# Performance work log

Measured on AMD Instinct MI355X. Metric: run time of the kernel, lower is better.

Reference implementation:

```python
import jax, jax.numpy as jnp
import numpy as np

B, S, H = 1, 4096, 2048
HQ, HKV, D = 8, 4, 256
WIN = 1024          # sliding window
SOFTCAP = 50.0      # attn logit softcapping
EPS = 1e-6          # rms_norm_eps
ROPE_THETA = 10000.0


def setup_inputs() -> dict:
    key = jax.random.key(0)
    ks = jax.random.split(key, 6)
    hidden_states = jax.random.normal(ks[0], (B, S, H), dtype=jnp.float32)
    # RoPE cos/sin tables, shape [B, S, D]
    inv_freq = 1.0 / (ROPE_THETA ** (jnp.arange(0, D, 2, dtype=jnp.float32) / D))
    pos = jnp.arange(S, dtype=jnp.float32)
    freqs = pos[:, None] * inv_freq[None, :]          # [S, D/2]
    emb = jnp.concatenate([freqs, freqs], axis=-1)    # [S, D]
    cos = jnp.broadcast_to(jnp.cos(emb)[None], (B, S, D)).astype(jnp.float32)
    sin = jnp.broadcast_to(jnp.sin(emb)[None], (B, S, D)).astype(jnp.float32)
    qpos = jnp.arange(S)[:, None]
    kpos = jnp.arange(S)[None, :]
    diff = qpos - kpos
    allowed = (diff >= 0) & (diff < WIN)
    attention_mask = jnp.where(allowed, 0.0, -1e9).astype(jnp.float32)[None, None]
    attention_mask = jnp.broadcast_to(attention_mask, (B, 1, S, S))
    w_scale = 0.02
    Wq = jax.random.normal(ks[1], (HQ * D, H), dtype=jnp.float32) * w_scale
    Wk = jax.random.normal(ks[2], (HKV * D, H), dtype=jnp.float32) * w_scale
    Wv = jax.random.normal(ks[3], (HKV * D, H), dtype=jnp.float32) * w_scale
    Wo = jax.random.normal(ks[4], (H, HQ * D), dtype=jnp.float32) * w_scale
    q_norm_w = jnp.ones((D,), dtype=jnp.float32)
    k_norm_w = jnp.ones((D,), dtype=jnp.float32)
    return {"hidden_states": hidden_states, "cos": cos, "sin": sin,
            "attention_mask": attention_mask, "Wq": Wq, "Wk": Wk, "Wv": Wv,
            "Wo": Wo, "q_norm_w": q_norm_w, "k_norm_w": k_norm_w}


def _rms_norm(x, weight=None):
    # Gemma4 RMSNorm in fp32: x * rsqrt(mean(x^2) + eps) [* weight]
    ms = jnp.mean(x * x, axis=-1, keepdims=True) + EPS
    y = x * jax.lax.rsqrt(ms)
    return y * weight if weight is not None else y


def _rope(x, cos, sin):
    # x: [B,S,Hn,D]; cos/sin: [B,S,D] -> unsqueeze at dim 2
    x1, x2 = jnp.split(x, 2, axis=-1)
    rot = jnp.concatenate([-x2, x1], axis=-1)
    return x * cos[:, :, None, :] + rot * sin[:, :, None, :]


def reference(hidden_states, cos, sin, attention_mask, Wq, Wk, Wv, Wo, q_norm_w, k_norm_w):
    n_rep = HQ // HKV
    q = (hidden_states @ Wq.T).reshape(B, S, HQ, D)     # [B,S,HQ,D]
    q = _rms_norm(q, q_norm_w)
    q = _rope(q, cos, sin).transpose(0, 2, 1, 3)        # [B,HQ,S,D]
    k = (hidden_states @ Wk.T).reshape(B, S, HKV, D)
    k = _rms_norm(k, k_norm_w)
    k = _rope(k, cos, sin).transpose(0, 2, 1, 3)        # [B,HKV,S,D]
    v = (hidden_states @ Wv.T).reshape(B, S, HKV, D)
    v = _rms_norm(v).transpose(0, 2, 1, 3)              # [B,HKV,S,D]
    # repeat_kv (GQA)
    k = jnp.repeat(k, n_rep, axis=1)                    # [B,HQ,S,D]
    v = jnp.repeat(v, n_rep, axis=1)
    scores = jnp.einsum('bhqd,bhkd->bhqk', q, k)        # scaling = 1.0
    scores = jnp.tanh(scores / SOFTCAP) * SOFTCAP       # softcap
    scores = scores + attention_mask
    attn = jax.nn.softmax(scores.astype(jnp.float32), axis=-1).astype(q.dtype)
    out = jnp.einsum('bhqk,bhkd->bhqd', attn, v)        # [B,HQ,S,D]
    out = out.transpose(0, 2, 1, 3).reshape(B, S, HQ * D)
    return out @ Wo.T                                   # [B,S,H]
```

## Files before the change

kernel.cpp:

```cpp
#include <hip/hip_runtime.h>

#define S_LEN 4096
#define HID   2048
#define NHQ   8
#define NKV   4
#define DHEAD 256
#define WIN   1024

typedef __attribute__((ext_vector_type(4))) float     floatx4;
typedef __attribute__((ext_vector_type(8))) _Float16  halfx8;
typedef __attribute__((ext_vector_type(8))) __bf16    bf16x8;

__device__ __forceinline__ unsigned short f2h(float f){
  union { _Float16 h; unsigned short u; } cv; cv.h = (_Float16)f; return cv.u;
}
__device__ __forceinline__ float h2f(unsigned short u){
  union { unsigned short u; _Float16 h; } cv; cv.u = u; return (float)cv.h;
}
__device__ __forceinline__ unsigned short f2bf(float f){
  unsigned int u = __float_as_uint(f);
  u += 0x7FFFu + ((u >> 16) & 1u);
  return (unsigned short)(u >> 16);
}

__device__ __forceinline__ void gld_lds16(const void* g, void* l){
  __builtin_amdgcn_global_load_lds((const __attribute__((address_space(1))) void*)g,
                                   (__attribute__((address_space(3))) void*)l, 16, 0, 0);
}

__global__ __launch_bounds__(256) void cvt_all(const float* __restrict__ hs,
                                               const float* __restrict__ Wq,
                                               const float* __restrict__ Wk,
                                               const float* __restrict__ Wv,
                                               const float* __restrict__ Wo,
                                               unsigned short* __restrict__ h_h,
                                               unsigned short* __restrict__ w_qkv,
                                               unsigned short* __restrict__ wo){
  int bid = blockIdx.x;
  const float* src;
  unsigned short* dst;
  size_t i;
  if (bid < 8192){
    i = ((size_t)bid * 256 + threadIdx.x) * 4;
    src = hs + i; dst = h_h + i;
  } else if (bid < 16384){
    i = ((size_t)(bid - 8192) * 256 + threadIdx.x) * 4;
    int row = (int)(i >> 11), col = (int)(i & 2047);
    src = ((row < 2048) ? (Wq + ((size_t)row << 11))
         : (row < 3072) ? (Wk + ((size_t)(row - 2048) << 11))
                        : (Wv + ((size_t)(row - 3072) << 11))) + col;
    dst = w_qkv + i;
  } else {
    i = ((size_t)(bid - 16384) * 256 + threadIdx.x) * 4;
    src = Wo + i; dst = wo + i;
  }
  float4 v = *(const float4*)src;
  *(ushort4*)dst = make_ushort4(f2h(v.x), f2h(v.y), f2h(v.z), f2h(v.w));
}

template<int OUT_F32>
__global__ __launch_bounds__(512, 2) void gemm_qkv8(const unsigned short* __restrict__ A,
                                                    const unsigned short* __restrict__ B,
                                                    void* __restrict__ Cv,
                                                    int ldC, int K, int nx){
  __shared__ __align__(16) unsigned short As[2][256 * 64];
  __shared__ __align__(16) unsigned short Bs[2][256 * 64];
  const int T = K >> 6;
  const int t0 = threadIdx.x, w = t0 >> 6, lane = t0 & 63;
  const int wm = w >> 2, wn = w & 3;
  const int quad = lane >> 4, l15 = lane & 15;
  const int r7 = l15 & 7;

  const int bid = (int)blockIdx.x;
  const int by = bid / nx, bx = bid - by * nx;
  const int bm0 = by * 256, bn0 = bx * 256;

  const int grow = lane >> 3;
  const int sg8  = (((lane & 7) ^ grow) << 3);

#define STGH(U, HALF)                                                          \
  {                                                                            \
    const int sl_ = (U) & 1;                                                   \
    const unsigned short* src_ = ((HALF) < 2)                                  \
        ? (A + (size_t)(bm0 + (((HALF) & 1) << 7)) * K)                        \
        : (B + (size_t)(bn0 + (((HALF) & 1) << 7)) * K);                       \
    unsigned short* dst_ = (((HALF) < 2) ? &As[sl_][0] : &Bs[sl_][0])          \
                           + ((((HALF) & 1) << 7) * 64);                       \
    _Pragma("unroll")                                                          \
    for (int L = 0; L < 2; ++L){                                               \
      const int ck = L * 8 + w;                                                \
      gld_lds16(src_ + (size_t)((ck << 3) + grow) * K + (size_t)(U) * 64 + sg8,\
                dst_ + ck * 512);                                              \
    }                                                                          \
  }

#define LDA(MI, KS) (*(const halfx8*)&Ap[(wm*128 + (MI)*16 + l15) * 64 + ((((KS)*4 + quad) ^ r7) << 3)])
#define LDB(NI, KS) (*(const halfx8*)&Bp[(wn*64  + (NI)*16 + l15) * 64 + ((((KS)*4 + quad) ^ r7) << 3)])

  STGH(0, 0) STGH(0, 1) STGH(0, 2) STGH(0, 3)
  asm volatile("s_waitcnt vmcnt(0)" ::: "memory");
  __builtin_amdgcn_s_barrier();

  const floatx4 zf = {0.f, 0.f, 0.f, 0.f};
  floatx4 acc[8][4];
#pragma unroll
  for (int mi = 0; mi < 8; ++mi)
#pragma unroll
    for (int ni = 0; ni < 4; ++ni) acc[mi][ni] = zf;

  for (int t = 0; t < T; ++t){
    const int cur = t & 1;
    const unsigned short* Ap = &As[cur][0];
    const unsigned short* Bp = &Bs[cur][0];
    const bool pf = (t + 1 < T);
    halfx8 af[4], bf0[4], bf1[4];

#pragma unroll
    for (int mi = 0; mi < 4; ++mi) af[mi] = LDA(mi, 0);
#pragma unroll
    for (int ni = 0; ni < 4; ++ni){ bf0[ni] = LDB(ni, 0); bf1[ni] = LDB(ni, 1); }
    if (pf) STGH(t + 1, 0)
    __builtin_amdgcn_s_barrier();
    asm volatile("s_waitcnt lgkmcnt(0)" ::: "memory");
    __builtin_amdgcn_sched_barrier(0);
    __builtin_amdgcn_s_setprio(1);
#pragma unroll
    for (int mi = 0; mi < 4; ++mi)
#pragma unroll
      for (int ni = 0; ni < 4; ++ni)
        acc[mi][ni] = __builtin_amdgcn_mfma_f32_16x16x32_f16(af[mi], bf0[ni], acc[mi][ni], 0, 0, 0);
    __builtin_amdgcn_s_setprio(0);
    __builtin_amdgcn_s_barrier();
    __builtin_amdgcn_sched_barrier(0);

#pragma unroll
    for (int mi = 0; mi < 4; ++mi) af[mi] = LDA(4 + mi, 0);
    if (pf) STGH(t + 1, 1)
    __builtin_amdgcn_s_barrier();
    asm volatile("s_waitcnt lgkmcnt(0)" ::: "memory");
    __builtin_amdgcn_sched_barrier(0);
    __builtin_amdgcn_s_setprio(1);
#pragma unroll
    for (int mi = 0; mi < 4; ++mi)
#pragma unroll
      for (int ni = 0; ni < 4; ++ni)
        acc[4 + mi][ni] = __builtin_amdgcn_mfma_f32_16x16x32_f16(af[mi], bf0[ni], acc[4 + mi][ni], 0, 0, 0);
    __builtin_amdgcn_s_setprio(0);
    __builtin_amdgcn_s_barrier();
    __builtin_amdgcn_sched_barrier(0);

#pragma unroll
    for (int mi = 0; mi < 4; ++mi) af[mi] = LDA(mi, 1);
    if (pf) STGH(t + 1, 2)
    __builtin_amdgcn_s_barrier();
    asm volatile("s_waitcnt lgkmcnt(0)" ::: "memory");
    __builtin_amdgcn_sched_barrier(0);
    __builtin_amdgcn_s_setprio(1);
#pragma unroll
    for (int mi = 0; mi < 4; ++mi)
#pragma unroll
      for (int ni = 0; ni < 4; ++ni)
        acc[mi][ni] = __builtin_amdgcn_mfma_f32_16x16x32_f16(af[mi], bf1[ni], acc[mi][ni], 0, 0, 0);
    __builtin_amdgcn_s_setprio(0);
    __builtin_amdgcn_s_barrier();
    __builtin_amdgcn_sched_barrier(0);

#pragma unroll
    for (int mi = 0; mi < 4; ++mi) af[mi] = LDA(4 + mi, 1);
    if (pf) STGH(t + 1, 3)
    __builtin_amdgcn_s_barrier();
    asm volatile("s_waitcnt lgkmcnt(0)" ::: "memory");
    __builtin_amdgcn_sched_barrier(0);
    __builtin_amdgcn_s_setprio(1);
#pragma unroll
    for (int mi = 0; mi < 4; ++mi)
#pragma unroll
      for (int ni = 0; ni < 4; ++ni)
        acc[4 + mi][ni] = __builtin_amdgcn_mfma_f32_16x16x32_f16(af[mi], bf1[ni], acc[4 + mi][ni], 0, 0, 0);
    __builtin_amdgcn_s_setprio(0);
    if (pf) { asm volatile("s_waitcnt vmcnt(0)" ::: "memory"); }
    __builtin_amdgcn_s_barrier();
    __builtin_amdgcn_sched_barrier(0);
  }
#undef STGH
#undef LDA
#undef LDB

#pragma unroll
  for (int mi = 0; mi < 8; ++mi)
#pragma unroll
    for (int ni = 0; ni < 4; ++ni)
#pragma unroll
      for (int r = 0; r < 4; ++r){
        int m = bm0 + wm*128 + mi*16 + quad*4 + r;
        int n = bn0 + wn*64 + ni*16 + l15;
        float v = acc[mi][ni][r];
        if (OUT_F32) ((float*)Cv)[(size_t)m * ldC + n] = v;
        else         ((unsigned short*)Cv)[(size_t)m * ldC + n] = f2h(v);
      }
}

__global__ __launch_bounds__(256) void qkv_post(const unsigned short* __restrict__ qkvh,
                                                const float* __restrict__ cosb,
                                                const float* __restrict__ sinb,
                                                const float* __restrict__ qnw,
                                                const float* __restrict__ knw,
                                                unsigned short* __restrict__ Qf,
                                                unsigned short* __restrict__ Kf,
                                                unsigned short* __restrict__ Vf){
  int gw   = blockIdx.x * 4 + (threadIdx.x >> 6);
  int lane = threadIdx.x & 63;
  int hh = gw & 15, s = gw >> 4;
  int colbase = (hh < 8) ? hh * 256 : (hh < 12 ? 2048 + (hh - 8) * 256 : 3072 + (hh - 12) * 256);

  ushort4 raw = *(const ushort4*)(qkvh + (size_t)s * 4096 + colbase + lane * 4);
  float x0 = h2f(raw.x), x1 = h2f(raw.y), x2 = h2f(raw.z), x3 = h2f(raw.w);
  float ss = x0*x0 + x1*x1 + x2*x2 + x3*x3;
#pragma unroll
  for (int off = 32; off; off >>= 1) ss += __shfl_xor(ss, off);
  float inv = rsqrtf(ss * (1.0f / 256.0f) + 1e-6f);

  if (hh < 12){
    const float* wp = (hh < 8) ? qnw : knw;
    float4 wv = *(const float4*)(wp + lane * 4);
    float y[4] = { x0*inv*wv.x, x1*inv*wv.y, x2*inv*wv.z, x3*inv*wv.w };
    float4 cv = *(const float4*)(cosb + (size_t)s * 256 + lane * 4);
    float4 sv = *(const float4*)(sinb + (size_t)s * 256 + lane * 4);
    float cj[4] = {cv.x, cv.y, cv.z, cv.w};
    float sj[4] = {sv.x, sv.y, sv.z, sv.w};
    unsigned short oh[4];
#pragma unroll
    for (int j = 0; j < 4; ++j){
      float oth = __shfl_xor(y[j], 32);
      float rot = (lane < 32) ? -oth : oth;
      oh[j] = f2h(y[j] * cj[j] + rot * sj[j]);
    }
    ushort4 r = make_ushort4(oh[0], oh[1], oh[2], oh[3]);
    if (hh < 8) *(ushort4*)(Qf + (size_t)(hh       * S_LEN + s) * DHEAD + lane * 4) = r;
    else        *(ushort4*)(Kf + (size_t)((hh - 8) * S_LEN + s) * DHEAD + lane * 4) = r;
  } else {
    ushort4 r = make_ushort4(f2bf(x0*inv), f2bf(x1*inv), f2bf(x2*inv), f2bf(x3*inv));
    *(ushort4*)(Vf + (size_t)((hh - 12) * S_LEN + s) * DHEAD + lane * 4) = r;
  }
}

__global__ __launch_bounds__(256) void transpose_v(const unsigned short* __restrict__ v,
                                                   unsigned short* __restrict__ vt){
  __shared__ unsigned short tile[64][68];
  int kv = blockIdx.z, d0 = blockIdx.x * 64, s0 = blockIdx.y * 64;
  int t = threadIdx.x;
  int r = t >> 4, c4 = (t & 15) * 4;
#pragma unroll
  for (int i = 0; i < 4; ++i){
    int row = r + i * 16;
    ushort4 xx = *(const ushort4*)(v + (size_t)(kv * S_LEN + s0 + row) * DHEAD + d0 + c4);
    tile[row][c4] = xx.x; tile[row][c4+1] = xx.y; tile[row][c4+2] = xx.z; tile[row][c4+3] = xx.w;
  }
  __syncthreads();
#pragma unroll
  for (int i = 0; i < 4; ++i){
    int dr = r + i * 16;
    ushort4 yy = make_ushort4(tile[c4][dr], tile[c4+1][dr], tile[c4+2][dr], tile[c4+3][dr]);
    *(ushort4*)(vt + (size_t)(kv * DHEAD + d0 + dr) * S_LEN + s0 + c4) = yy;
  }
}

__global__ __launch_bounds__(256, 1) void attn_win(const unsigned short* __restrict__ Qg,
                                                   const unsigned short* __restrict__ Kg,
                                                   const unsigned short* __restrict__ Vt,
                                                   unsigned short* __restrict__ Og){
  __shared__ __align__(16) unsigned short Ks[2][8 * 32 * 32];
  __shared__ __align__(16) unsigned short Vts[2][256 * 32];
  __shared__ __align__(16) unsigned short Pb[4][32 * 40];

  const int bid = blockIdx.x;
  const int h = bid & 7, kv = h >> 1;
  const int q0 = (bid >> 3) * 128;
  const int t = threadIdx.x, w = t >> 6, lane = t & 63;
  const int quad = lane >> 4, l15 = lane & 15;
  const int l2 = lane >> 2;
  const int gsw = (((lane & 3) ^ ((l2 >> 1) & 3)) << 3);
  const int qsw = ((quad ^ ((l15 >> 1) & 3)) << 3);
  const int qw0 = q0 + w * 32;

  halfx8 qf[2][8];
#pragma unroll
  for (int s = 0; s < 2; ++s)
#pragma unroll
    for (int c = 0; c < 8; ++c)
      qf[s][c] = *(const halfx8*)(Qg + (size_t)(h * S_LEN + qw0 + s*16 + l15) * DHEAD + c*32 + quad*8);

  const floatx4 zf = {0.f, 0.f, 0.f, 0.f};
  floatx4 oacc[2][16];
#pragma unroll
  for (int s = 0; s < 2; ++s)
#pragma unroll
    for (int dt = 0; dt < 16; ++dt) oacc[s][dt] = zf;
  float l_part[2][4] = {{0.f,0.f,0.f,0.f},{0.f,0.f,0.f,0.f}};

  int kt_lo = q0 / 32 - 32; if (kt_lo < 0) kt_lo = 0;
  int kt_hi = q0 / 32 + 3;

  const size_t kbase = (size_t)kv * S_LEN * DHEAD;
  const size_t vbase = (size_t)kv * DHEAD * S_LEN;

#define STAGE(KT, B)                                                              \
  {                                                                               \
    const int key0_ = (KT) * 32;                                                  \
    _Pragma("unroll")                                                             \
    for (int j = 0; j < 4; ++j){                                                  \
      int ch = j * 4 + w;                                                         \
      int krow = (ch & 1) * 16 + l2;                                              \
      int cb = ch >> 1;                                                           \
      gld_lds16(Kg + kbase + (size_t)(key0_ + krow) * DHEAD + cb * 32 + gsw,      \
                &Ks[B][ch * 512]);                                                \
      int drow = ch * 16 + l2;                                                    \
      gld_lds16(Vt + vbase + (size_t)drow * S_LEN + key0_ + gsw,                  \
                &Vts[B][ch * 512]);                                               \
    }                                                                             \
  }

  STAGE(kt_lo, 0);

  for (int kt = kt_lo; kt <= kt_hi; ++kt){
    const int cur = (kt - kt_lo) & 1;
    if (kt < kt_hi){
      STAGE(kt + 1, cur ^ 1);
      asm volatile("s_waitcnt vmcnt(8)" ::: "memory");
    } else {
      asm volatile("s_waitcnt vmcnt(0)" ::: "memory");
    }
    __builtin_amdgcn_s_barrier();

    const int key0 = kt * 32;
    if (key0 <= qw0 + 31 && key0 + 31 >= qw0 - (WIN - 1)){
      floatx4 sc[2][2];
      sc[0][0] = zf; sc[0][1] = zf; sc[1][0] = zf; sc[1][1] = zf;
      __builtin_amdgcn_s_setprio(1);
#pragma unroll
      for (int c = 0; c < 8; ++c){
#pragma unroll
        for (int nt = 0; nt < 2; ++nt){
          halfx8 kf = *(const halfx8*)&Ks[cur][c * 1024 + (nt*16 + l15) * 32 + qsw];
          sc[0][nt] = __builtin_amdgcn_mfma_f32_16x16x32_f16(qf[0][c], kf, sc[0][nt], 0, 0, 0);
          sc[1][nt] = __builtin_amdgcn_mfma_f32_16x16x32_f16(qf[1][c], kf, sc[1][nt], 0, 0, 0);
        }
      }
      __builtin_amdgcn_s_setprio(0);
      const bool tfull = (key0 + 31 <= qw0) && (qw0 + 31 - key0 < WIN);
#pragma unroll
      for (int s = 0; s < 2; ++s)
#pragma unroll
        for (int nt = 0; nt < 2; ++nt)
#pragma unroll
          for (int r = 0; r < 4; ++r){
            float v = sc[s][nt][r];
            float e  = __builtin_amdgcn_exp2f(v * 0.0577078016f);
            float tt = __builtin_amdgcn_rcpf(e + 1.0f);
            float p  = __builtin_amdgcn_exp2f(fmaf(tt, -144.26950408f, 28.8539008f));
            if (!tfull){
              int qi = qw0 + s*16 + quad*4 + r;
              int ki = key0 + nt*16 + l15;
              p = ((ki <= qi) && (qi - ki < WIN)) ? p : 0.0f;
            }
            l_part[s][r] += p;
            Pb[w][(s*16 + quad*4 + r) * 40 + nt*16 + l15] = f2bf(p);
          }
      bf16x8 pf0 = *(const bf16x8*)&Pb[w][l15 * 40 + quad * 8];
      bf16x8 pf1 = *(const bf16x8*)&Pb[w][(16 + l15) * 40 + quad * 8];
      __builtin_amdgcn_s_setprio(1);
#pragma unroll
      for (int dt = 0; dt < 16; ++dt){
        bf16x8 vf = *(const bf16x8*)&Vts[cur][(dt*16 + l15) * 32 + qsw];
        oacc[0][dt] = __builtin_amdgcn_mfma_f32_16x16x32_bf16(pf0, vf, oacc[0][dt], 0, 0, 0);
        oacc[1][dt] = __builtin_amdgcn_mfma_f32_16x16x32_bf16(pf1, vf, oacc[1][dt], 0, 0, 0);
      }
      __builtin_amdgcn_s_setprio(0);
    }
    __builtin_amdgcn_s_barrier();
  }
#undef STAGE

#pragma unroll
  for (int s = 0; s < 2; ++s)
#pragma unroll
    for (int r = 0; r < 4; ++r){
      float l = l_part[s][r];
      l += __shfl_xor(l, 1);
      l += __shfl_xor(l, 2);
      l += __shfl_xor(l, 4);
      l += __shfl_xor(l, 8);
      float rl = 1.0f / l;
      int srow = qw0 + s*16 + quad*4 + r;
#pragma unroll
      for (int dt = 0; dt < 16; ++dt)
        Og[(size_t)srow * (NHQ * DHEAD) + h * DHEAD + dt*16 + l15] = f2h(oacc[s][dt][r] * rl);
    }
}

extern "C" void kernel_launch(void* const* d_in, const int* in_sizes, int n_in,
                              void* d_out, int out_size, void* d_ws, size_t ws_size,
                              hipStream_t stream){
  const float* hs   = (const float*)d_in[0];
  const float* cosb = (const float*)d_in[1];
  const float* sinb = (const float*)d_in[2];
  const float* Wq   = (const float*)d_in[4];
  const float* Wk   = (const float*)d_in[5];
  const float* Wv   = (const float*)d_in[6];
  const float* Wo   = (const float*)d_in[7];
  const float* qnw  = (const float*)d_in[8];
  const float* knw  = (const float*)d_in[9];
  float* out = (float*)d_out;

  const size_t MB = 1024ull * 1024ull;
  char* ws = (char*)d_ws;
  unsigned short* h_h   = (unsigned short*)(ws);
  unsigned short* w_qkv = (unsigned short*)(ws + 16 * MB);
  unsigned short* wo    = (unsigned short*)(ws + 32 * MB);
  unsigned short* qkvh  = (unsigned short*)(ws + 40 * MB);
  unsigned short* Qf    = (unsigned short*)(ws);
  unsigned short* Kf    = (unsigned short*)(ws + 16 * MB);
  unsigned short* Vf    = (unsigned short*)(ws + 24 * MB);
  unsigned short* vt    = (unsigned short*)(ws + 40 * MB);
  unsigned short* ob    = (unsigned short*)(ws + 48 * MB);

  cvt_all<<<20480, 256, 0, stream>>>(hs, Wq, Wk, Wv, Wo, h_h, w_qkv, wo);

  gemm_qkv8<0><<<256, 512, 0, stream>>>(h_h, w_qkv, qkvh, 4096, 2048, 16);

  qkv_post<<<16384, 256, 0, stream>>>(qkvh, cosb, sinb, qnw, knw, Qf, Kf, Vf);
  transpose_v<<<dim3(4, 64, 4), 256, 0, stream>>>(Vf, vt);

  attn_win<<<256, 256, 0, stream>>>(Qf, Kf, vt, ob);

  gemm_qkv8<1><<<128, 512, 0, stream>>>(ob, wo, out, 2048, 2048, 8);
}
```

Baseline: 431.0 us.

## Split attention key range across two blocks and merge partial outputs

The windowed attention kernel is split along the key dimension: each query tile is handled by two blocks covering halves of the key tiles, giving 512 blocks instead of 256 to fill more CUs. Each half writes a normalized fp16 output plus its row sums, and a new merge kernel combines them weighted by the row sums. Because softmax uses a fixed max (softcap bound), the partials can be merged without rescaling. A fallback 512-thread attention variant is used when workspace is small. The cost is an extra kernel launch and an extra round trip of the attention output through memory.

```diff
diff --git a/kernel.cpp b/kernel.cpp
--- a/kernel.cpp
+++ b/kernel.cpp
@@ -265,17 +265,20 @@
   }
 }
 
-__global__ __launch_bounds__(256, 1) void attn_win(const unsigned short* __restrict__ Qg,
-                                                   const unsigned short* __restrict__ Kg,
-                                                   const unsigned short* __restrict__ Vt,
-                                                   unsigned short* __restrict__ Og){
+__global__ __launch_bounds__(256, 1) void attn_sp(const unsigned short* __restrict__ Qg,
+                                                  const unsigned short* __restrict__ Kg,
+                                                  const unsigned short* __restrict__ Vt,
+                                                  unsigned short* __restrict__ Oh,
+                                                  float* __restrict__ lh){
   __shared__ __align__(16) unsigned short Ks[2][8 * 32 * 32];
   __shared__ __align__(16) unsigned short Vts[2][256 * 32];
   __shared__ __align__(16) unsigned short Pb[4][32 * 40];
 
   const int bid = blockIdx.x;
   const int h = bid & 7, kv = h >> 1;
-  const int q0 = (bid >> 3) * 128;
+  const int rest = bid >> 3;
+  const int q0 = (rest >> 1) * 128;
+  const int half = rest & 1;
   const int t = threadIdx.x, w = t >> 6, lane = t & 63;
   const int quad = lane >> 4, l15 = lane & 15;
   const int l2 = lane >> 2;
@@ -298,8 +301,11 @@
     for (int dt = 0; dt < 16; ++dt) oacc[s][dt] = zf;
   float l_part[2][4] = {{0.f,0.f,0.f,0.f},{0.f,0.f,0.f,0.f}};
 
-  int kt_lo = q0 / 32 - 32; if (kt_lo < 0) kt_lo = 0;
-  int kt_hi = q0 / 32 + 3;
+  int lo = q0 / 32 - 32; if (lo < 0) lo = 0;
+  const int hi = q0 / 32 + 3;
+  const int mid = lo + ((hi - lo + 2) >> 1);
+  const int lo_h = half ? mid : lo;
+  const int hi_h = half ? hi : mid - 1;
 
   const size_t kbase = (size_t)kv * S_LEN * DHEAD;
   const size_t vbase = (size_t)kv * DHEAD * S_LEN;
@@ -320,11 +326,11 @@
     }                                                                             \
   }
 
-  STAGE(kt_lo, 0);
-
-  for (int kt = kt_lo; kt <= kt_hi; ++kt){
-    const int cur = (kt - kt_lo) & 1;
-    if (kt < kt_hi){
+  STAGE(lo_h, 0);
+
+  for (int kt = lo_h; kt <= hi_h; ++kt){
+    const int cur = (kt - lo_h) & 1;
+    if (kt < hi_h){
       STAGE(kt + 1, cur ^ 1);
       asm volatile("s_waitcnt vmcnt(8)" ::: "memory");
     } else {
@@ -381,6 +387,7 @@
   }
 #undef STAGE
 
+  const size_t obase = (size_t)half * (8ull << 20);
 #pragma unroll
   for (int s = 0; s < 2; ++s)
 #pragma unroll
@@ -390,12 +397,154 @@
       l += __shfl_xor(l, 2);
       l += __shfl_xor(l, 4);
       l += __shfl_xor(l, 8);
-      float rl = 1.0f / l;
+      float rl = (l > 0.f) ? (1.0f / l) : 0.f;
       int srow = qw0 + s*16 + quad*4 + r;
+      if (l15 == 0) lh[((size_t)half * NHQ + h) * S_LEN + srow] = l;
 #pragma unroll
       for (int dt = 0; dt < 16; ++dt)
-        Og[(size_t)srow * (NHQ * DHEAD) + h * DHEAD + dt*16 + l15] = f2h(oacc[s][dt][r] * rl);
+        Oh[obase + (size_t)srow * (NHQ * DHEAD) + h * DHEAD + dt*16 + l15] = f2h(oacc[s][dt][r] * rl);
     }
+}
+
+__global__ __launch_bounds__(256) void merge_o(unsigned short* __restrict__ Oab,
+                                               const float* __restrict__ lh){
+  size_t i = ((size_t)blockIdx.x * 256 + threadIdx.x) * 4;
+  int row = (int)(i >> 11);
+  int h   = (int)((i & 2047) >> 8);
+  float a = lh[(size_t)h * S_LEN + row];
+  float b = lh[((size_t)NHQ + h) * S_LEN + row];
+  float wsum = 1.0f / (a + b);
+  float wa = a * wsum, wb = b * wsum;
+  ushort4 xa = *(const ushort4*)(Oab + i);
+  ushort4 xb = *(const ushort4*)(Oab + (8ull << 20) + i);
+  ushort4 o = make_ushort4(
+    f2h(h2f(xa.x) * wa + h2f(xb.x) * wb),
+    f2h(h2f(xa.y) * wa + h2f(xb.y) * wb),
+    f2h(h2f(xa.z) * wa + h2f(xb.z) * wb),
+    f2h(h2f(xa.w) * wa + h2f(xb.w) * wb));
+  *(ushort4*)(Oab + i) = o;
+}
+
+__global__ __launch_bounds__(512, 2) void attn_win(const unsigned short* __restrict__ Qg,
+                                                   const unsigned short* __restrict__ Kg,
+                                                   const unsigned short* __restrict__ Vt,
+                                                   unsigned short* __restrict__ Og){
+  __shared__ __align__(16) unsigned short Ks[2][8 * 32 * 32];
+  __shared__ __align__(16) unsigned short Vts[2][256 * 32];
+  __shared__ __align__(16) unsigned short Pb[8][16 * 40];
+
+  const int bid = blockIdx.x;
+  const int h = bid & 7, kv = h >> 1;
+  const int q0 = (bid >> 3) * 128;
+  const int t = threadIdx.x, w = t >> 6, lane = t & 63;
+  const int quad = lane >> 4, l15 = lane & 15;
+  const int l2 = lane >> 2;
+  const int gsw = (((lane & 3) ^ ((l2 >> 1) & 3)) << 3);
+  const int qsw = ((quad ^ ((l15 >> 1) & 3)) << 3);
+  const int qw0 = q0 + w * 16;
+
+  halfx8 qf[8];
+#pragma unroll
+  for (int c = 0; c < 8; ++c)
+    qf[c] = *(const halfx8*)(Qg + (size_t)(h * S_LEN + qw0 + l15) * DHEAD + c*32 + quad*8);
+
+  const floatx4 zf = {0.f, 0.f, 0.f, 0.f};
+  floatx4 oacc[16];
+#pragma unroll
+  for (int dt = 0; dt < 16; ++dt) oacc[dt] = zf;
+  float l_part[4] = {0.f, 0.f, 0.f, 0.f};
+
+  int kt_lo = q0 / 32 - 32; if (kt_lo < 0) kt_lo = 0;
+  int kt_hi = q0 / 32 + 3;
+
+  const size_t kbase = (size_t)kv * S_LEN * DHEAD;
+  const size_t vbase = (size_t)kv * DHEAD * S_LEN;
+
+#define STAGE(KT, B)                                                              \
+  {                                                                               \
+    const int key0_ = (KT) * 32;                                                  \
+    _Pragma("unroll")                                                             \
+    for (int j = 0; j < 2; ++j){                                                  \
+      int ch = j * 8 + w;                                                         \
+      int krow = (ch & 1) * 16 + l2;                                              \
+      int cb = ch >> 1;                                                           \
+      gld_lds16(Kg + kbase + (size_t)(key0_ + krow) * DHEAD + cb * 32 + gsw,      \
+                &Ks[B][ch * 512]);                                                \
+      int drow = ch * 16 + l2;                                                    \
+      gld_lds16(Vt + vbase + (size_t)drow * S_LEN + key0_ + gsw,                  \
+                &Vts[B][ch * 512]);                                               \
+    }                                                                             \
+  }
+
+  STAGE(kt_lo, 0);
+
+  for (int kt = kt_lo; kt <= kt_hi; ++kt){
+    const int cur = (kt - kt_lo) & 1;
+    if (kt < kt_hi){
+      STAGE(kt + 1, cur ^ 1);
+      asm volatile("s_waitcnt vmcnt(4)" ::: "memory");
+    } else {
+      asm volatile("s_waitcnt vmcnt(0)" ::: "memory");
+    }
+    __builtin_amdgcn_s_barrier();
+
+    const int key0 = kt * 32;
+    if (key0 <= qw0 + 15 && key0 + 31 >= qw0 - (WIN - 1)){
+      floatx4 sc[2];
+      sc[0] = zf; sc[1] = zf;
+      __builtin_amdgcn_s_setprio(1);
+#pragma unroll
+      for (int c = 0; c < 8; ++c){
+#pragma unroll
+        for (int nt = 0; nt < 2; ++nt){
+          halfx8 kf = *(const halfx8*)&Ks[cur][c * 1024 + (nt*16 + l15) * 32 + qsw];
+          sc[nt] = __builtin_amdgcn_mfma_f32_16x16x32_f16(qf[c], kf, sc[nt], 0, 0, 0);
+        }
+      }
+      __builtin_amdgcn_s_setprio(0);
+      const bool tfull = (key0 + 31 <= qw0) && (qw0 + 15 - key0 < WIN);
+#pragma unroll
+      for (int nt = 0; nt < 2; ++nt)
+#pragma unroll
+        for (int r = 0; r < 4; ++r){
+          float v = sc[nt][r];
+          float e  = __builtin_amdgcn_exp2f(v * 0.0577078016f);
+          float tt = __builtin_amdgcn_rcpf(e + 1.0f);
+          float p  = __builtin_amdgcn_exp2f(fmaf(tt, -144.26950408f, 28.8539008f));
+          if (!tfull){
+            int qi = qw0 + quad*4 + r;
+            int ki = key0 + nt*16 + l15;
+            p = ((ki <= qi) && (qi - ki < WIN)) ? p : 0.0f;
+          }
+          l_part[r] += p;
+          Pb[w][(quad*4 + r) * 40 + nt*16 + l15] = f2bf(p);
+        }
+      bf16x8 pf = *(const bf16x8*)&Pb[w][l15 * 40 + quad * 8];
+      __builtin_amdgcn_s_setprio(1);
+#pragma unroll
+      for (int dt = 0; dt < 16; ++dt){
+        bf16x8 vf = *(const bf16x8*)&Vts[cur][(dt*16 + l15) * 32 + qsw];
+        oacc[dt] = __builtin_amdgcn_mfma_f32_16x16x32_bf16(pf, vf, oacc[dt], 0, 0, 0);
+      }
+      __builtin_amdgcn_s_setprio(0);
+    }
+    __builtin_amdgcn_s_barrier();
+  }
+#undef STAGE
+
+#pragma unroll
+  for (int r = 0; r < 4; ++r){
+    float l = l_part[r];
+    l += __shfl_xor(l, 1);
+    l += __shfl_xor(l, 2);
+    l += __shfl_xor(l, 4);
+    l += __shfl_xor(l, 8);
+    float rl = 1.0f / l;
+    int srow = qw0 + quad*4 + r;
+#pragma unroll
+    for (int dt = 0; dt < 16; ++dt)
+      Og[(size_t)srow * (NHQ * DHEAD) + h * DHEAD + dt*16 + l15] = f2h(oacc[dt][r] * rl);
+  }
 }
 
 extern "C" void kernel_launch(void* const* d_in, const int* in_sizes, int n_in,
@@ -423,6 +572,8 @@
   unsigned short* Vf    = (unsigned short*)(ws + 24 * MB);
   unsigned short* vt    = (unsigned short*)(ws + 40 * MB);
   unsigned short* ob    = (unsigned short*)(ws + 48 * MB);
+  unsigned short* obB   = (unsigned short*)(ws + 64 * MB);
+  float*          lab   = (float*)(ws + 80 * MB);
 
   cvt_all<<<20480, 256, 0, stream>>>(hs, Wq, Wk, Wv, Wo, h_h, w_qkv, wo);
 
@@ -431,7 +582,12 @@
   qkv_post<<<16384, 256, 0, stream>>>(qkvh, cosb, sinb, qnw, knw, Qf, Kf, Vf);
   transpose_v<<<dim3(4, 64, 4), 256, 0, stream>>>(Vf, vt);
 
-  attn_win<<<256, 256, 0, stream>>>(Qf, Kf, vt, ob);
+  if (ws_size >= 81 * MB) {
+    attn_sp<<<512, 256, 0, stream>>>(Qf, Kf, vt, ob, lab);
+    merge_o<<<8192, 256, 0, stream>>>(ob, lab);
+  } else {
+    attn_win<<<256, 512, 0, stream>>>(Qf, Kf, vt, ob);
+  }
 
   gemm_qkv8<1><<<128, 512, 0, stream>>>(ob, wo, out, 2048, 2048, 8);
 }
```

Result: no change. 439.5 us (+2.0%).
